# Performance work log

Hardware: AMD Instinct MI355X
Metric: run time of the kernel (lower is better)

Reference implementation:

```python
import jax, jax.numpy as jnp
import numpy as np

N, E = 100000, 1600000
NFEAT, NHID, NCLASS, NLAYER = 128, 128, 40, 3


def _glorot(key, shape):
    fan_in, fan_out = shape[0], shape[1]
    lim = float(np.sqrt(6.0 / (fan_in + fan_out)))
    return jax.random.uniform(key, shape, jnp.float32, -lim, lim)


def setup_inputs() -> dict:
    key = jax.random.key(0)
    ks = jax.random.split(key, 12)
    x = jax.random.normal(ks[0], (N, NFEAT), jnp.float32)
    src = jax.random.randint(ks[1], (E,), 0, N, jnp.int32)
    dst = jax.random.randint(ks[2], (E,), 0, N, jnp.int32)
    W1 = _glorot(ks[3], (NFEAT, NHID)); b1 = jnp.zeros((NHID,), jnp.float32)
    W2 = _glorot(ks[4], (NHID, NHID)); b2 = jnp.zeros((NHID,), jnp.float32)
    Wg = jnp.stack([_glorot(ks[5 + l], (NHID, NHID)) for l in range(NLAYER)])  # [L,H,H]
    bg = jnp.zeros((NLAYER, NHID), jnp.float32)
    Wc = _glorot(ks[5 + NLAYER], (NHID, NCLASS)); bc = jnp.zeros((NCLASS,), jnp.float32)
    return {"x": x, "src": src, "dst": dst, "W1": W1, "b1": b1, "W2": W2,
            "b2": b2, "Wg": Wg, "bg": bg, "Wc": Wc, "bc": bc}


def _graph_conv(h, src, dst, W, b, out_norm, in_norm):
    # DGL GraphConv norm='both': scale by src out-deg^{-1/2}, sum-aggregate,
    # scale by dst in-deg^{-1/2}, then linear (in_feats == out_feats -> W after agg).
    h = h * out_norm[:, None]
    agg = jax.ops.segment_sum(h[src], dst, num_segments=N)
    return (agg * in_norm[:, None]) @ W + b


def reference(x, src, dst, W1, b1, W2, b2, Wg, bg, Wc, bc):
    ones = jnp.ones((E,), jnp.float32)
    out_deg = jnp.clip(jax.ops.segment_sum(ones, src, num_segments=N), 1.0)
    in_deg = jnp.clip(jax.ops.segment_sum(ones, dst, num_segments=N), 1.0)
    out_norm = jax.lax.rsqrt(out_deg)
    in_norm = jax.lax.rsqrt(in_deg)

    h = x @ W1 + b1            # feature1
    h = h @ W2 + b2            # feature2
    for l in range(NLAYER):    # stacked GraphConv + ReLU (dropout is identity in eval)
        h = _graph_conv(h, src, dst, Wg[l], bg[l], out_norm, in_norm)
        h = jax.nn.relu(h)
    return h @ Wc + bc         # classifier
```

## Files before the change

kernel.cpp:

```cpp
#include <hip/hip_runtime.h>
#include <hip/hip_fp16.h>
#include <cstdint>
#include <cstddef>

constexpr int NN  = 100000;
constexpr int EE  = 1600000;
constexpr int HID = 128;
constexpr int BUK = 256;
constexpr int NBUK = (NN + BUK - 1) / BUK;
constexpr int BLKE = 2048;
constexpr int NBE  = (EE + BLKE - 1) / BLKE;
constexpr int MH   = NBUK * NBE;
constexpr int MH2  = 2 * MH;
constexpr int NSC  = (MH2 + 2047) / 2048;

typedef float f32x4_t __attribute__((ext_vector_type(4)));
typedef short bf16x8_t __attribute__((ext_vector_type(8)));

static __device__ __forceinline__ short f2bf(float f) {
    union { float f; unsigned u; } x; x.f = f;
    unsigned r = x.u + 0x7FFF + ((x.u >> 16) & 1);
    return (short)(r >> 16);
}
static __device__ __forceinline__ float bf2f(short b) {
    union { unsigned u; float f; } x; x.u = ((unsigned)(unsigned short)b) << 16;
    return x.f;
}

__global__ __launch_bounds__(256) void bh_both_k(const int* __restrict__ src, const int* __restrict__ dst,
                                                 int* __restrict__ bh2) {
    __shared__ int hd[NBUK], hs[NBUK];
    int blk = blockIdx.x, t = threadIdx.x;
    for (int i = t; i < NBUK; i += 256) { hd[i] = 0; hs[i] = 0; }
    __syncthreads();
    int e0 = blk * BLKE, e1 = min(e0 + BLKE, EE);
    for (int e = e0 + t; e < e1; e += 256) {
        atomicAdd(&hd[dst[e] >> 8], 1);
        atomicAdd(&hs[src[e] >> 8], 1);
    }
    __syncthreads();
    for (int i = t; i < NBUK; i += 256) {
        bh2[i * NBE + blk]      = hd[i];
        bh2[MH + i * NBE + blk] = hs[i];
    }
}

__global__ __launch_bounds__(256) void scan_sum_k(const int* __restrict__ in, int* __restrict__ bsum, int n) {
    __shared__ int sc[256];
    int b = blockIdx.x, t = threadIdx.x;
    int base = b * 2048 + t * 8;
    int s = 0;
#pragma unroll
    for (int j = 0; j < 8; j++) { int idx = base + j; s += (idx < n) ? in[idx] : 0; }
    sc[t] = s; __syncthreads();
    for (int off = 128; off > 0; off >>= 1) {
        if (t < off) sc[t] += sc[t + off];
        __syncthreads();
    }
    if (t == 0) bsum[b] = sc[0];
}

__global__ __launch_bounds__(512) void scan_top_k(const int* __restrict__ bsum, int* __restrict__ boff, int nb) {
    __shared__ int sc[512];
    int t = threadIdx.x;
    int v = (t < nb) ? bsum[t] : 0;
    sc[t] = v; __syncthreads();
    for (int off = 1; off < 512; off <<= 1) {
        int u = (t >= off) ? sc[t - off] : 0;
        __syncthreads();
        sc[t] += u;
        __syncthreads();
    }
    if (t < nb) boff[t] = sc[t] - v;
}

__global__ __launch_bounds__(256) void scan_chunk_k(const int* __restrict__ in, const int* __restrict__ boff,
                                                    int* __restrict__ out, int n) {
    __shared__ int sc[256];
    int b = blockIdx.x, t = threadIdx.x;
    int base = b * 2048 + t * 8;
    int c[8];
    int s = 0;
#pragma unroll
    for (int j = 0; j < 8; j++) { int idx = base + j; c[j] = (idx < n) ? in[idx] : 0; s += c[j]; }
    sc[t] = s; __syncthreads();
    for (int off = 1; off < 256; off <<= 1) {
        int v = (t >= off) ? sc[t - off] : 0;
        __syncthreads();
        sc[t] += v;
        __syncthreads();
    }
    int excl = sc[t] - s + boff[b];
#pragma unroll
    for (int j = 0; j < 8; j++) {
        int idx = base + j;
        if (idx < n) out[idx] = excl;
        excl += c[j];
    }
}

__global__ __launch_bounds__(256) void scatter_both_k(const int* __restrict__ src, const int* __restrict__ dst,
                                                      const int* __restrict__ off2,
                                                      unsigned* __restrict__ pairs, unsigned char* __restrict__ sbyte) {
    __shared__ int cd[NBUK], cs[NBUK];
    int blk = blockIdx.x, t = threadIdx.x;
    for (int i = t; i < NBUK; i += 256) {
        cd[i] = off2[i * NBE + blk];
        cs[i] = off2[MH + i * NBE + blk] - EE;
    }
    __syncthreads();
    int e0 = blk * BLKE, e1 = min(e0 + BLKE, EE);
    for (int e = e0 + t; e < e1; e += 256) {
        int d = dst[e], s = src[e];
        int pd = atomicAdd(&cd[d >> 8], 1);
        pairs[pd] = ((unsigned)(d & 255) << 17) | (unsigned)s;
        int ps = atomicAdd(&cs[s >> 8], 1);
        sbyte[ps] = (unsigned char)(s & 255);
    }
}

__global__ __launch_bounds__(512) void bucket_csr_ocnt_k(
    const unsigned* __restrict__ pairs, const unsigned char* __restrict__ sbyte,
    const int* __restrict__ off2,
    int* __restrict__ rowptr, int* __restrict__ col,
    float* __restrict__ inorm, float* __restrict__ onorm) {
    __shared__ int hist[BUK];
    __shared__ int excl[BUK];
    __shared__ int psum[BUK];
    int t = threadIdx.x;

    if (blockIdx.x >= NBUK) {
        int b = blockIdx.x - NBUK;
        int base = off2[MH + b * NBE] - EE;
        int endv = (b == NBUK - 1) ? EE : off2[MH + (b + 1) * NBE] - EE;
        if (t < BUK) hist[t] = 0;
        __syncthreads();
        for (int i = base + t; i < endv; i += 512) atomicAdd(&hist[sbyte[i]], 1);
        __syncthreads();
        if (t < BUK) {
            int node = b * BUK + t;
            if (node < NN) {
                int c = hist[t]; if (c < 1) c = 1;
                onorm[node] = rsqrtf((float)c);
            }
        }
        return;
    }

    int b = blockIdx.x;
    int base = off2[b * NBE];
    int endv = (b == NBUK - 1) ? EE : off2[(b + 1) * NBE];
    if (t < BUK) hist[t] = 0;
    __syncthreads();
    for (int i = base + t; i < endv; i += 512) atomicAdd(&hist[pairs[i] >> 17], 1);
    __syncthreads();
    int ps = 0;
    if (t < BUK) { ps = hist[t]; psum[t] = ps; }
    __syncthreads();
    for (int off = 1; off < BUK; off <<= 1) {
        int u = 0;
        if (t < BUK && t >= off) u = psum[t - off];
        __syncthreads();
        if (t < BUK) psum[t] += u;
        __syncthreads();
    }
    if (t < BUK) {
        int pex = psum[t] - ps;
        excl[t] = pex;
        int node = b * BUK + t;
        if (node < NN) {
            rowptr[node] = base + pex;
            int c = ps; if (c < 1) c = 1;
            inorm[node] = rsqrtf((float)c);
        }
    }
    if (b == NBUK - 1 && t == 0) rowptr[NN] = EE;
    __syncthreads();
    for (int i = base + t; i < endv; i += 512) {
        unsigned p = pairs[i];
        int pos = base + atomicAdd(&excl[p >> 17], 1);
        col[pos] = (int)(p & 0x1FFFFu);
    }
}

__global__ __launch_bounds__(256) void w12_k(const float* __restrict__ W1, const float* __restrict__ W2,
                                             const float* __restrict__ b1, const float* __restrict__ b2,
                                             const float* __restrict__ Wg,
                                             float* __restrict__ W12, float* __restrict__ b12,
                                             short* __restrict__ wsp) {
    int t = threadIdx.x;
    if (blockIdx.x == 65) {
        const float* W = Wg + 2 * 128 * 128;
        short* Bh = wsp;
        short* Bl = wsp + 16384;
        for (int j = 0; j < 16; j++) {
            int fi = (j * 256 + t) * 4;
            int k = fi >> 7, n0 = fi & 127;
            float4 wv = *(const float4*)(W + fi);
            float wa[4] = {wv.x, wv.y, wv.z, wv.w};
#pragma unroll
            for (int cc = 0; cc < 4; cc++) {
                int g = n0 + cc;
                int q2 = g >> 2;
                int ntc = q2 & 7;
                int c = ((q2 >> 3) << 2) | (g & 3);
                int kblk = k >> 5, ksub = k & 31;
                int lane_ = ((ksub >> 3) << 4) | c;
                int sidx = ((ntc * 4 + kblk) * 64 + lane_) * 8 + (ksub & 7);
                short hi = f2bf(wa[cc]);
                Bh[sidx] = hi; Bl[sidx] = f2bf(wa[cc] - bf2f(hi));
            }
        }
        return;
    }
    if (blockIdx.x == 64) {
        int j = t;
        if (j < 128) {
            float acc = b2[j];
            for (int k = 0; k < 128; k++) acc = fmaf(b1[k], W2[k * 128 + j], acc);
            b12[j] = acc;
        }
        return;
    }
    int idx = blockIdx.x * 256 + t;
    int i = idx >> 7, j = idx & 127;
    float a0 = 0.f, a1 = 0.f, a2 = 0.f, a3 = 0.f;
    for (int k = 0; k < 128; k += 4) {
        a0 = fmaf(W1[i * 128 + k],     W2[(k)     * 128 + j], a0);
        a1 = fmaf(W1[i * 128 + k + 1], W2[(k + 1) * 128 + j], a1);
        a2 = fmaf(W1[i * 128 + k + 2], W2[(k + 2) * 128 + j], a2);
        a3 = fmaf(W1[i * 128 + k + 3], W2[(k + 3) * 128 + j], a3);
    }
    W12[idx] = (a0 + a1) + (a2 + a3);
}

__global__ __launch_bounds__(256) void agg_k(const float4* __restrict__ h16, const int* __restrict__ rowptr,
                                             const int* __restrict__ col, const float* __restrict__ inorm,
                                             short* __restrict__ h0h, short* __restrict__ h0l) {
    int w = (int)((blockIdx.x * 256 + threadIdx.x) >> 6);
    if (w >= NN) return;
    int lane = threadIdx.x & 63;
    int q   = lane >> 4;
    int l16 = lane & 15;
    int beg = rowptr[w], end = rowptr[w + 1];
    float acc[8];
#pragma unroll
    for (int j = 0; j < 8; j++) acc[j] = 0.f;

    union HU { float4 f4; __half2 h2[4]; };
    int i = beg + q;
    for (; i + 12 < end; i += 16) {
        int s0 = col[i], s1 = col[i + 4], s2 = col[i + 8], s3 = col[i + 12];
        HU u0, u1, u2, u3;
        u0.f4 = h16[(size_t)s0 * 16 + l16];
        u1.f4 = h16[(size_t)s1 * 16 + l16];
        u2.f4 = h16[(size_t)s2 * 16 + l16];
        u3.f4 = h16[(size_t)s3 * 16 + l16];
#pragma unroll
        for (int p = 0; p < 4; p++) {
            float2 a = __half22float2(u0.h2[p]);
            float2 b = __half22float2(u1.h2[p]);
            float2 c = __half22float2(u2.h2[p]);
            float2 d = __half22float2(u3.h2[p]);
            acc[2 * p]     += (a.x + b.x) + (c.x + d.x);
            acc[2 * p + 1] += (a.y + b.y) + (c.y + d.y);
        }
    }
    for (; i < end; i += 4) {
        int s = col[i];
        HU u; u.f4 = h16[(size_t)s * 16 + l16];
#pragma unroll
        for (int p = 0; p < 4; p++) {
            float2 a = __half22float2(u.h2[p]);
            acc[2 * p]     += a.x;
            acc[2 * p + 1] += a.y;
        }
    }
#pragma unroll
    for (int mm = 16; mm <= 32; mm <<= 1)
#pragma unroll
        for (int j = 0; j < 8; j++) acc[j] += __shfl_xor(acc[j], mm);
    if (q == 0) {
        float s = inorm[w];
        bf16x8_t hv, lv;
#pragma unroll
        for (int j = 0; j < 8; j++) {
            float v = acc[j] * s;
            short hi = f2bf(v);
            hv[j] = hi;
            lv[j] = f2bf(v - bf2f(hi));
        }
        *(bf16x8_t*)&h0h[(size_t)w * 128 + l16 * 8] = hv;
        *(bf16x8_t*)&h0l[(size_t)w * 128 + l16 * 8] = lv;
    }
}

template <int NT, bool RELU, bool OUTSCALE, bool OUTHALF, bool INSPLIT>
__global__ __launch_bounds__(256) void mfma_gemm_k(
    const void* __restrict__ in, const short* __restrict__ inl,
    const float* __restrict__ W, const float* __restrict__ bias,
    void* __restrict__ outp, const float* __restrict__ outscale,
    int nrows, int ncols, int ntiles) {

    __shared__ short Bh[NT * 2048];
    __shared__ short Bl[NT * 2048];
    __shared__ __half Tr[OUTHALF ? 4 * 16 * 128 : 1];

    const int t = threadIdx.x;

    if constexpr (NT == 8) {
        for (int j = 0; j < 16; j++) {
            int fi = (j * 256 + t) * 4;
            int k = fi >> 7, n0 = fi & 127;
            float4 wv = *(const float4*)(W + fi);
            float wa[4] = {wv.x, wv.y, wv.z, wv.w};
#pragma unroll
            for (int cc = 0; cc < 4; cc++) {
                int g = n0 + cc;
                int q2 = g >> 2;
                int ntc = q2 & 7;
                int c = ((q2 >> 3) << 2) | (g & 3);
                int kblk = k >> 5, ksub = k & 31;
                int lane_ = ((ksub >> 3) << 4) | c;
                int sidx = ((ntc * 4 + kblk) * 64 + lane_) * 8 + (ksub & 7);
                short hi = f2bf(wa[cc]);
                Bh[sidx] = hi; Bl[sidx] = f2bf(wa[cc] - bf2f(hi));
            }
        }
    } else {
        for (int idx = t; idx < 128 * 64; idx += 256) {
            int k = idx >> 6, g = idx & 63;
            if (g < NT * 16) {
                float w = (g < 40) ? ((const float*)W)[k * 40 + g] : 0.f;
                int q2 = g >> 2;
                int ntc = q2 % NT;
                int c = (q2 / NT) * 4 + (g & 3);
                int kblk = k >> 5, ksub = k & 31;
                int lane_ = ((ksub >> 3) << 4) | c;
                int sidx = ((ntc * 4 + kblk) * 64 + lane_) * 8 + (ksub & 7);
                short hi = f2bf(w);
                Bh[sidx] = hi; Bl[sidx] = f2bf(w - bf2f(hi));
            }
        }
    }
    __syncthreads();

    const int wave = t >> 6;
    const int lane = t & 63;
    const int m    = lane & 15;
    const int kq   = lane >> 4;
    const int cbase = kq * 4 * NT;

    float bstat[4 * NT];
#pragma unroll
    for (int i = 0; i < 4 * NT; i++) {
        int g = cbase + i;
        bstat[i] = (g < ncols) ? bias[g] : 0.f;
    }

    const int wstride = gridDim.x * 4;
    for (int tile = blockIdx.x * 4 + wave; tile < ntiles; tile += wstride) {
        int row = tile * 16 + m;
        bool rv = row < nrows;

        bf16x8_t Ah[4], Al[4];
        if constexpr (INSPLIT) {
            const short* ih = (const short*)in + (size_t)row * 128 + kq * 8;
            const short* il = inl + (size_t)row * 128 + kq * 8;
#pragma unroll
            for (int kb = 0; kb < 4; kb++) {
                if (rv) {
                    Ah[kb] = *(const bf16x8_t*)(ih + kb * 32);
                    Al[kb] = *(const bf16x8_t*)(il + kb * 32);
                } else {
                    Ah[kb] = (bf16x8_t){0,0,0,0,0,0,0,0};
                    Al[kb] = (bf16x8_t){0,0,0,0,0,0,0,0};
                }
            }
        } else {
#pragma unroll
            for (int kb = 0; kb < 4; kb++) {
                const float* ap = (const float*)in + (size_t)row * 128 + kb * 32 + kq * 8;
                float4 p0, p1;
                if (rv) { p0 = *(const float4*)ap; p1 = *(const float4*)(ap + 4); }
                else    { p0 = make_float4(0,0,0,0); p1 = make_float4(0,0,0,0); }
                float av[8] = {p0.x, p0.y, p0.z, p0.w, p1.x, p1.y, p1.z, p1.w};
#pragma unroll
                for (int j = 0; j < 8; j++) {
                    float v = av[j];
                    short hi = f2bf(v);
                    Ah[kb][j] = hi;
                    Al[kb][j] = f2bf(v - bf2f(hi));
                }
            }
        }

        float osc = 1.f;
        if (OUTSCALE && rv) osc = outscale[row];

        float ov[4 * NT] __attribute__((aligned(16)));
#pragma unroll
        for (int nt = 0; nt < NT; nt++) {
            f32x4_t acc = {0.f, 0.f, 0.f, 0.f};
#pragma unroll
            for (int kb = 0; kb < 4; kb++) {
                const bf16x8_t bh = *(const bf16x8_t*)&Bh[((nt * 4 + kb) * 64 + lane) * 8];
                const bf16x8_t bl = *(const bf16x8_t*)&Bl[((nt * 4 + kb) * 64 + lane) * 8];
                acc = __builtin_amdgcn_mfma_f32_16x16x32_bf16(bh, Ah[kb], acc, 0, 0, 0);
                acc = __builtin_amdgcn_mfma_f32_16x16x32_bf16(bh, Al[kb], acc, 0, 0, 0);
                acc = __builtin_amdgcn_mfma_f32_16x16x32_bf16(bl, Ah[kb], acc, 0, 0, 0);
            }
#pragma unroll
            for (int r = 0; r < 4; r++) {
                float v = acc[r] + bstat[nt * 4 + r];
                if (RELU) v = fmaxf(v, 0.f);
                ov[nt * 4 + r] = v * osc;
            }
        }

        if constexpr (OUTHALF) {
            __half* tw = &Tr[wave * 2048];
#pragma unroll
            for (int p = 0; p < 4; p++) {
                union { __half h[8]; float4 f4; } U;
#pragma unroll
                for (int j = 0; j < 8; j++) U.h[j] = __float2half_rn(ov[p * 8 + j]);
                int bo = (cbase * 2 + p * 16) ^ ((m & 7) << 4);
                *(float4*)((char*)(tw + m * 128) + bo) = U.f4;
            }
#pragma unroll
            for (int s2 = 0; s2 < 4; s2++) {
                int r = s2 * 4 + (lane >> 4);
                int bo = ((lane & 15) * 16) ^ ((r & 7) << 4);
                float4 v = *(const float4*)((char*)(tw + r * 128) + bo);
                *(float4*)((__half*)outp + (size_t)(tile * 16 + r) * ncols + (lane & 15) * 8) = v;
            }
        } else if (rv) {
            if constexpr (NT == 8) {
                float4* p = (float4*)((float*)outp + (size_t)row * 128 + cbase);
#pragma unroll
                for (int j = 0; j < 8; j++) p[j] = ((const float4*)ov)[j];
            } else {
                float* p = (float*)outp + (size_t)row * 40 + cbase;
#pragma unroll
                for (int j = 0; j < 3; j++) {
                    if (cbase + j * 4 < 40) *(float4*)(p + j * 4) = ((const float4*)ov)[j];
                }
            }
        }
    }
}

__global__ __launch_bounds__(256) void conv_cls_k(
    const short* __restrict__ inh, const short* __restrict__ inl,
    const short* __restrict__ gBh, const short* __restrict__ gBl,
    const float* __restrict__ bg2,
    const float* __restrict__ Wc, const float* __restrict__ bc,
    float* __restrict__ out, int ntiles) {

    __shared__ short WcH[3 * 2048];
    __shared__ short WcL[3 * 2048];
    __shared__ short Lh[4][16][136];
    __shared__ short Ll[4][16][136];

    const int t = threadIdx.x;

    for (int idx = t; idx < 128 * 64; idx += 256) {
        int k = idx >> 6, g = idx & 63;
        if (g < 48) {
            float w = (g < 40) ? Wc[k * 40 + g] : 0.f;
            int q2 = g >> 2;
            int ntc = q2 % 3;
            int c = (q2 / 3) * 4 + (g & 3);
            int kblk = k >> 5, ksub = k & 31;
            int lane_ = ((ksub >> 3) << 4) | c;
            int sidx = ((ntc * 4 + kblk) * 64 + lane_) * 8 + (ksub & 7);
            short hi = f2bf(w);
            WcH[sidx] = hi; WcL[sidx] = f2bf(w - bf2f(hi));
        }
    }
    __syncthreads();

    const int wave = t >> 6;
    const int lane = t & 63;
    const int m    = lane & 15;
    const int kq   = lane >> 4;
    const int cbase = kq * 32;
    const int cbc   = kq * 12;

    float bstat[32];
#pragma unroll
    for (int i = 0; i < 32; i++) bstat[i] = bg2[cbase + i];
    float bstatC[12];
#pragma unroll
    for (int i = 0; i < 12; i++) {
        int g = cbc + i;
        bstatC[i] = (g < 40) ? bc[g] : 0.f;
    }

    const int wstride = gridDim.x * 4;
    for (int tile = blockIdx.x * 4 + wave; tile < ntiles; tile += wstride) {
        const int row = tile * 16 + m;

        bf16x8_t Ah[4], Al[4];
        {
            const short* ih = inh + (size_t)row * 128 + kq * 8;
            const short* il = inl + (size_t)row * 128 + kq * 8;
#pragma unroll
            for (int kb = 0; kb < 4; kb++) {
                Ah[kb] = *(const bf16x8_t*)(ih + kb * 32);
                Al[kb] = *(const bf16x8_t*)(il + kb * 32);
            }
        }

        float ov[32] __attribute__((aligned(16)));
#pragma unroll
        for (int nt = 0; nt < 8; nt++) {
            f32x4_t acc = {0.f, 0.f, 0.f, 0.f};
#pragma unroll
            for (int kb = 0; kb < 4; kb++) {
                const bf16x8_t bh = *(const bf16x8_t*)&gBh[((nt * 4 + kb) * 64 + lane) * 8];
                const bf16x8_t bl = *(const bf16x8_t*)&gBl[((nt * 4 + kb) * 64 + lane) * 8];
                acc = __builtin_amdgcn_mfma_f32_16x16x32_bf16(bh, Ah[kb], acc, 0, 0, 0);
                acc = __builtin_amdgcn_mfma_f32_16x16x32_bf16(bh, Al[kb], acc, 0, 0, 0);
                acc = __builtin_amdgcn_mfma_f32_16x16x32_bf16(bl, Ah[kb], acc, 0, 0, 0);
            }
#pragma unroll
            for (int r = 0; r < 4; r++) {
                float v = acc[r] + bstat[nt * 4 + r];
                ov[nt * 4 + r] = fmaxf(v, 0.f);
            }
        }

#pragma unroll
        for (int p = 0; p < 4; p++) {
            bf16x8_t hv, lv;
#pragma unroll
            for (int j = 0; j < 8; j++) {
                float v = ov[p * 8 + j];
                short hi = f2bf(v);
                hv[j] = hi;
                lv[j] = f2bf(v - bf2f(hi));
            }
            *(bf16x8_t*)&Lh[wave][m][cbase + p * 8] = hv;
            *(bf16x8_t*)&Ll[wave][m][cbase + p * 8] = lv;
        }

        float ovc[12] __attribute__((aligned(16)));
#pragma unroll
        for (int ntc = 0; ntc < 3; ntc++) {
            f32x4_t acc = {0.f, 0.f, 0.f, 0.f};
#pragma unroll
            for (int kb = 0; kb < 4; kb++) {
                const bf16x8_t wh = *(const bf16x8_t*)&WcH[((ntc * 4 + kb) * 64 + lane) * 8];
                const bf16x8_t wl = *(const bf16x8_t*)&WcL[((ntc * 4 + kb) * 64 + lane) * 8];
                const bf16x8_t fh = *(const bf16x8_t*)&Lh[wave][m][kb * 32 + kq * 8];
                const bf16x8_t fl = *(const bf16x8_t*)&Ll[wave][m][kb * 32 + kq * 8];
                acc = __builtin_amdgcn_mfma_f32_16x16x32_bf16(wh, fh, acc, 0, 0, 0);
                acc = __builtin_amdgcn_mfma_f32_16x16x32_bf16(wh, fl, acc, 0, 0, 0);
                acc = __builtin_amdgcn_mfma_f32_16x16x32_bf16(wl, fh, acc, 0, 0, 0);
            }
#pragma unroll
            for (int r = 0; r < 4; r++) ovc[ntc * 4 + r] = acc[r] + bstatC[ntc * 4 + r];
        }

        float* p = out + (size_t)row * 40 + cbc;
#pragma unroll
        for (int j = 0; j < 3; j++) {
            if (cbc + j * 4 < 40) *(float4*)(p + j * 4) = ((const float4*)ovc)[j];
        }
    }
}

extern "C" void kernel_launch(void* const* d_in, const int* in_sizes, int n_in,
                              void* d_out, int out_size, void* d_ws, size_t ws_size,
                              hipStream_t stream) {
    const float* x   = (const float*)d_in[0];
    const int*   src = (const int*)d_in[1];
    const int*   dst = (const int*)d_in[2];
    const float* W1  = (const float*)d_in[3];
    const float* b1  = (const float*)d_in[4];
    const float* W2  = (const float*)d_in[5];
    const float* b2  = (const float*)d_in[6];
    const float* Wg  = (const float*)d_in[7];
    const float* bg  = (const float*)d_in[8];
    const float* Wc  = (const float*)d_in[9];
    const float* bc  = (const float*)d_in[10];
    float* out = (float*)d_out;

    char* ws = (char*)d_ws;
    size_t off = 0;
    auto alloc = [&](size_t bytes) -> void* {
        void* p = ws + off;
        off += (bytes + 255) & ~(size_t)255;
        return p;
    };
    short*  h0h    = (short*)alloc((size_t)NN * HID * 2);
    short*  h0l    = (short*)alloc((size_t)NN * HID * 2);
    __half* h16    = (__half*)alloc((size_t)NN * HID * 2);
    float*  W12    = (float*)alloc(128 * 128 * 4);
    float*  b12    = (float*)alloc(128 * 4);
    short*  wsp    = (short*)alloc(2 * 16384 * 2);
    float*  onorm  = (float*)alloc((size_t)NN * 4);
    float*  inorm  = (float*)alloc((size_t)NN * 4);
    int*    rowptr = (int*)alloc((size_t)(NN + 1) * 4);
    int*    col    = (int*)alloc((size_t)EE * 4);
    int*    bh2    = (int*)alloc((size_t)MH2 * 4);
    int*    off2   = (int*)alloc((size_t)MH2 * 4);
    int*    bsum   = (int*)alloc((size_t)NSC * 4);
    int*    boff   = (int*)alloc((size_t)NSC * 4);
    unsigned*      pairs = (unsigned*)h0h;
    unsigned char* sbyte = (unsigned char*)h0h + (size_t)EE * 4;

    bh_both_k<<<NBE, 256, 0, stream>>>(src, dst, bh2);
    scan_sum_k<<<NSC, 256, 0, stream>>>(bh2, bsum, MH2);
    scan_top_k<<<1, 512, 0, stream>>>(bsum, boff, NSC);
    scan_chunk_k<<<NSC, 256, 0, stream>>>(bh2, boff, off2, MH2);
    scatter_both_k<<<NBE, 256, 0, stream>>>(src, dst, off2, pairs, sbyte);
    bucket_csr_ocnt_k<<<2 * NBUK, 512, 0, stream>>>(pairs, sbyte, off2,
                                                    rowptr, col, inorm, onorm);

    w12_k<<<66, 256, 0, stream>>>(W1, W2, b1, b2, Wg, W12, b12, wsp);

    const int ntiles = NN / 16;
    const int ggrid  = 512;

    mfma_gemm_k<8, false, true, true, false><<<ggrid, 256, 0, stream>>>(
        x, nullptr, W12, b12, h16, onorm, NN, 128, ntiles);
    for (int l = 0; l < 3; l++) {
        agg_k<<<(NN * 64 + 255) / 256, 256, 0, stream>>>(
            (const float4*)h16, rowptr, col, inorm, h0h, h0l);
        if (l < 2) {
            mfma_gemm_k<8, true, true, true, true><<<ggrid, 256, 0, stream>>>(
                h0h, h0l, Wg + (size_t)l * 128 * 128, bg + (size_t)l * 128, h16, onorm, NN, 128, ntiles);
        } else {
            conv_cls_k<<<ggrid, 256, 0, stream>>>(
                h0h, h0l, wsp, wsp + 16384, bg + 2 * 128, Wc, bc, out, ntiles);
        }
    }
}
```

Baseline: 534.7 us.

## Process two 16-row tiles per wave in the MFMA GEMM to reuse B fragments

The generic GEMM kernel is specialised to the 128-column fp16-output case, and each wave now handles 32 rows (two 16-row tiles) per iteration. Each B fragment read from LDS then feeds six MFMAs instead of three, which halves LDS traffic per output. The grid changes to 391 blocks with launch_bounds(256,2). In exchange register pressure rises from the doubled A fragments and accumulators, and row bounds checks are dropped, which relies on NN being divisible by 32.

```diff
diff --git a/kernel.cpp b/kernel.cpp
--- a/kernel.cpp
+++ b/kernel.cpp
@@ -295,52 +295,35 @@
     }
 }
 
-template <int NT, bool RELU, bool OUTSCALE, bool OUTHALF, bool INSPLIT>
-__global__ __launch_bounds__(256) void mfma_gemm_k(
+template <bool RELU, bool INSPLIT>
+__global__ __launch_bounds__(256, 2) void mfma_gemm2_k(
     const void* __restrict__ in, const short* __restrict__ inl,
     const float* __restrict__ W, const float* __restrict__ bias,
-    void* __restrict__ outp, const float* __restrict__ outscale,
-    int nrows, int ncols, int ntiles) {
-
-    __shared__ short Bh[NT * 2048];
-    __shared__ short Bl[NT * 2048];
-    __shared__ __half Tr[OUTHALF ? 4 * 16 * 128 : 1];
+    __half* __restrict__ outp, const float* __restrict__ outscale,
+    int nst) {
+
+    __shared__ short Bh[8 * 2048];
+    __shared__ short Bl[8 * 2048];
+    __shared__ __half Tr[4 * 16 * 128];
 
     const int t = threadIdx.x;
 
-    if constexpr (NT == 8) {
-        for (int j = 0; j < 16; j++) {
-            int fi = (j * 256 + t) * 4;
-            int k = fi >> 7, n0 = fi & 127;
-            float4 wv = *(const float4*)(W + fi);
-            float wa[4] = {wv.x, wv.y, wv.z, wv.w};
-#pragma unroll
-            for (int cc = 0; cc < 4; cc++) {
-                int g = n0 + cc;
-                int q2 = g >> 2;
-                int ntc = q2 & 7;
-                int c = ((q2 >> 3) << 2) | (g & 3);
-                int kblk = k >> 5, ksub = k & 31;
-                int lane_ = ((ksub >> 3) << 4) | c;
-                int sidx = ((ntc * 4 + kblk) * 64 + lane_) * 8 + (ksub & 7);
-                short hi = f2bf(wa[cc]);
-                Bh[sidx] = hi; Bl[sidx] = f2bf(wa[cc] - bf2f(hi));
-            }
-        }
-    } else {
-        for (int idx = t; idx < 128 * 64; idx += 256) {
-            int k = idx >> 6, g = idx & 63;
-            if (g < NT * 16) {
-                float w = (g < 40) ? ((const float*)W)[k * 40 + g] : 0.f;
-                int q2 = g >> 2;
-                int ntc = q2 % NT;
-                int c = (q2 / NT) * 4 + (g & 3);
-                int kblk = k >> 5, ksub = k & 31;
-                int lane_ = ((ksub >> 3) << 4) | c;
-                int sidx = ((ntc * 4 + kblk) * 64 + lane_) * 8 + (ksub & 7);
-                short hi = f2bf(w);
-                Bh[sidx] = hi; Bl[sidx] = f2bf(w - bf2f(hi));
-            }
+    for (int j = 0; j < 16; j++) {
+        int fi = (j * 256 + t) * 4;
+        int k = fi >> 7, n0 = fi & 127;
+        float4 wv = *(const float4*)(W + fi);
+        float wa[4] = {wv.x, wv.y, wv.z, wv.w};
+#pragma unroll
+        for (int cc = 0; cc < 4; cc++) {
+            int g = n0 + cc;
+            int q2 = g >> 2;
+            int ntc = q2 & 7;
+            int c = ((q2 >> 3) << 2) | (g & 3);
+            int kblk = k >> 5, ksub = k & 31;
+            int lane_ = ((ksub >> 3) << 4) | c;
+            int sidx = ((ntc * 4 + kblk) * 64 + lane_) * 8 + (ksub & 7);
+            short hi = f2bf(wa[cc]);
+            Bh[sidx] = hi; Bl[sidx] = f2bf(wa[cc] - bf2f(hi));
         }
     }
     __syncthreads();
@@ -349,104 +332,110 @@
     const int lane = t & 63;
     const int m    = lane & 15;
     const int kq   = lane >> 4;
-    const int cbase = kq * 4 * NT;
-
-    float bstat[4 * NT];
-#pragma unroll
-    for (int i = 0; i < 4 * NT; i++) {
-        int g = cbase + i;
-        bstat[i] = (g < ncols) ? bias[g] : 0.f;
-    }
+    const int cbase = kq * 32;
+
+    float bstat[32];
+#pragma unroll
+    for (int i = 0; i < 32; i++) bstat[i] = bias[cbase + i];
 
     const int wstride = gridDim.x * 4;
-    for (int tile = blockIdx.x * 4 + wave; tile < ntiles; tile += wstride) {
-        int row = tile * 16 + m;
-        bool rv = row < nrows;
-
-        bf16x8_t Ah[4], Al[4];
+    for (int st = blockIdx.x * 4 + wave; st < nst; st += wstride) {
+        const int row0 = st * 32 + m;
+        const int row1 = row0 + 16;
+
+        bf16x8_t A0h[4], A0l[4], A1h[4], A1l[4];
         if constexpr (INSPLIT) {
-            const short* ih = (const short*)in + (size_t)row * 128 + kq * 8;
-            const short* il = inl + (size_t)row * 128 + kq * 8;
+            const short* ih0 = (const short*)in + (size_t)row0 * 128 + kq * 8;
+            const short* il0 = inl + (size_t)row0 * 128 + kq * 8;
 #pragma unroll
             for (int kb = 0; kb < 4; kb++) {
-                if (rv) {
-                    Ah[kb] = *(const bf16x8_t*)(ih + kb * 32);
-                    Al[kb] = *(const bf16x8_t*)(il + kb * 32);
-                } else {
-                    Ah[kb] = (bf16x8_t){0,0,0,0,0,0,0,0};
-                    Al[kb] = (bf16x8_t){0,0,0,0,0,0,0,0};
+                A0h[kb] = *(const bf16x8_t*)(ih0 + kb * 32);
+                A0l[kb] = *(const bf16x8_t*)(il0 + kb * 32);
+                A1h[kb] = *(const bf16x8_t*)(ih0 + 2048 + kb * 32);
+                A1l[kb] = *(const bf16x8_t*)(il0 + 2048 + kb * 32);
+            }
+        } else {
+#pragma unroll
+            for (int kb = 0; kb < 4; kb++) {
+                const float* ap0 = (const float*)in + (size_t)row0 * 128 + kb * 32 + kq * 8;
+                float4 p0 = *(const float4*)ap0;
+                float4 p1 = *(const float4*)(ap0 + 4);
+                float4 p2 = *(const float4*)(ap0 + 2048);
+                float4 p3 = *(const float4*)(ap0 + 2048 + 4);
+                float a0v[8] = {p0.x, p0.y, p0.z, p0.w, p1.x, p1.y, p1.z, p1.w};
+                float a1v[8] = {p2.x, p2.y, p2.z, p2.w, p3.x, p3.y, p3.z, p3.w};
+#pragma unroll
+                for (int j = 0; j < 8; j++) {
+                    short h0_ = f2bf(a0v[j]);
+                    A0h[kb][j] = h0_;
+                    A0l[kb][j] = f2bf(a0v[j] - bf2f(h0_));
+                    short h1_ = f2bf(a1v[j]);
+                    A1h[kb][j] = h1_;
+                    A1l[kb][j] = f2bf(a1v[j] - bf2f(h1_));
                 }
             }
-        } else {
-#pragma unroll
-            for (int kb = 0; kb < 4; kb++) {
-                const float* ap = (const float*)in + (size_t)row * 128 + kb * 32 + kq * 8;
-                float4 p0, p1;
-                if (rv) { p0 = *(const float4*)ap; p1 = *(const float4*)(ap + 4); }
-                else    { p0 = make_float4(0,0,0,0); p1 = make_float4(0,0,0,0); }
-                float av[8] = {p0.x, p0.y, p0.z, p0.w, p1.x, p1.y, p1.z, p1.w};
-#pragma unroll
-                for (int j = 0; j < 8; j++) {
-                    float v = av[j];
-                    short hi = f2bf(v);
-                    Ah[kb][j] = hi;
-                    Al[kb][j] = f2bf(v - bf2f(hi));
-                }
-            }
-        }
-
-        float osc = 1.f;
-        if (OUTSCALE && rv) osc = outscale[row];
-
-        float ov[4 * NT] __attribute__((aligned(16)));
-#pragma unroll
-        for (int nt = 0; nt < NT; nt++) {
-            f32x4_t acc = {0.f, 0.f, 0.f, 0.f};
+        }
+
+        const float osc0 = outscale[row0];
+        const float osc1 = outscale[row1];
+
+        float ov0[32] __attribute__((aligned(16)));
+        float ov1[32] __attribute__((aligned(16)));
+#pragma unroll
+        for (int nt = 0; nt < 8; nt++) {
+            f32x4_t a0 = {0.f, 0.f, 0.f, 0.f};
+            f32x4_t a1 = {0.f, 0.f, 0.f, 0.f};
 #pragma unroll
             for (int kb = 0; kb < 4; kb++) {
                 const bf16x8_t bh = *(const bf16x8_t*)&Bh[((nt * 4 + kb) * 64 + lane) * 8];
                 const bf16x8_t bl = *(const bf16x8_t*)&Bl[((nt * 4 + kb) * 64 + lane) * 8];
-                acc = __builtin_amdgcn_mfma_f32_16x16x32_bf16(bh, Ah[kb], acc, 0, 0, 0);
-                acc = __builtin_amdgcn_mfma_f32_16x16x32_bf16(bh, Al[kb], acc, 0, 0, 0);
-                acc = __builtin_amdgcn_mfma_f32_16x16x32_bf16(bl, Ah[kb], acc, 0, 0, 0);
+                a0 = __builtin_amdgcn_mfma_f32_16x16x32_bf16(bh, A0h[kb], a0, 0, 0, 0);
+                a0 = __builtin_amdgcn_mfma_f32_16x16x32_bf16(bh, A0l[kb], a0, 0, 0, 0);
+                a0 = __builtin_amdgcn_mfma_f32_16x16x32_bf16(bl, A0h[kb], a0, 0, 0, 0);
+                a1 = __builtin_amdgcn_mfma_f32_16x16x32_bf16(bh, A1h[kb], a1, 0, 0, 0);
+                a1 = __builtin_amdgcn_mfma_f32_16x16x32_bf16(bh, A1l[kb], a1, 0, 0, 0);
+                a1 = __builtin_amdgcn_mfma_f32_16x16x32_bf16(bl, A1h[kb], a1, 0, 0, 0);
             }
 #pragma unroll
             for (int r = 0; r < 4; r++) {
-                float v = acc[r] + bstat[nt * 4 + r];
-                if (RELU) v = fmaxf(v, 0.f);
-                ov[nt * 4 + r] = v * osc;
-            }
-        }
-
-        if constexpr (OUTHALF) {
-            __half* tw = &Tr[wave * 2048];
-#pragma unroll
-            for (int p = 0; p < 4; p++) {
-                union { __half h[8]; float4 f4; } U;
-#pragma unroll
-                for (int j = 0; j < 8; j++) U.h[j] = __float2half_rn(ov[p * 8 + j]);
-                int bo = (cbase * 2 + p * 16) ^ ((m & 7) << 4);
-                *(float4*)((char*)(tw + m * 128) + bo) = U.f4;
-            }
-#pragma unroll
-            for (int s2 = 0; s2 < 4; s2++) {
-                int r = s2 * 4 + (lane >> 4);
-                int bo = ((lane & 15) * 16) ^ ((r & 7) << 4);
-                float4 v = *(const float4*)((char*)(tw + r * 128) + bo);
-                *(float4*)((__half*)outp + (size_t)(tile * 16 + r) * ncols + (lane & 15) * 8) = v;
-            }
-        } else if (rv) {
-            if constexpr (NT == 8) {
-                float4* p = (float4*)((float*)outp + (size_t)row * 128 + cbase);
-#pragma unroll
-                for (int j = 0; j < 8; j++) p[j] = ((const float4*)ov)[j];
-            } else {
-                float* p = (float*)outp + (size_t)row * 40 + cbase;
-#pragma unroll
-                for (int j = 0; j < 3; j++) {
-                    if (cbase + j * 4 < 40) *(float4*)(p + j * 4) = ((const float4*)ov)[j];
-                }
-            }
+                float v0 = a0[r] + bstat[nt * 4 + r];
+                float v1 = a1[r] + bstat[nt * 4 + r];
+                if (RELU) { v0 = fmaxf(v0, 0.f); v1 = fmaxf(v1, 0.f); }
+                ov0[nt * 4 + r] = v0 * osc0;
+                ov1[nt * 4 + r] = v1 * osc1;
+            }
+        }
+
+        __half* tw = &Tr[wave * 2048];
+#pragma unroll
+        for (int p = 0; p < 4; p++) {
+            union { __half h[8]; float4 f4; } U;
+#pragma unroll
+            for (int j = 0; j < 8; j++) U.h[j] = __float2half_rn(ov0[p * 8 + j]);
+            int bo = (cbase * 2 + p * 16) ^ ((m & 7) << 4);
+            *(float4*)((char*)(tw + m * 128) + bo) = U.f4;
+        }
+#pragma unroll
+        for (int s2 = 0; s2 < 4; s2++) {
+            int r = s2 * 4 + (lane >> 4);
+            int bo = ((lane & 15) * 16) ^ ((r & 7) << 4);
+            float4 v = *(const float4*)((char*)(tw + r * 128) + bo);
+            *(float4*)(outp + (size_t)(st * 32 + r) * 128 + (lane & 15) * 8) = v;
+        }
+#pragma unroll
+        for (int p = 0; p < 4; p++) {
+            union { __half h[8]; float4 f4; } U;
+#pragma unroll
+            for (int j = 0; j < 8; j++) U.h[j] = __float2half_rn(ov1[p * 8 + j]);
+            int bo = (cbase * 2 + p * 16) ^ ((m & 7) << 4);
+            *(float4*)((char*)(tw + m * 128) + bo) = U.f4;
+        }
+#pragma unroll
+        for (int s2 = 0; s2 < 4; s2++) {
+            int r = s2 * 4 + (lane >> 4);
+            int bo = ((lane & 15) * 16) ^ ((r & 7) << 4);
+            float4 v = *(const float4*)((char*)(tw + r * 128) + bo);
+            *(float4*)(outp + (size_t)(st * 32 + 16 + r) * 128 + (lane & 15) * 8) = v;
         }
     }
 }
@@ -623,18 +612,19 @@
     w12_k<<<66, 256, 0, stream>>>(W1, W2, b1, b2, Wg, W12, b12, wsp);
 
     const int ntiles = NN / 16;
-    const int ggrid  = 512;
-
-    mfma_gemm_k<8, false, true, true, false><<<ggrid, 256, 0, stream>>>(
-        x, nullptr, W12, b12, h16, onorm, NN, 128, ntiles);
+    const int nst    = NN / 32;
+    const int g2grid = 391;
+
+    mfma_gemm2_k<false, false><<<g2grid, 256, 0, stream>>>(
+        x, nullptr, W12, b12, h16, onorm, nst);
     for (int l = 0; l < 3; l++) {
         agg_k<<<(NN * 64 + 255) / 256, 256, 0, stream>>>(
             (const float4*)h16, rowptr, col, inorm, h0h, h0l);
         if (l < 2) {
-            mfma_gemm_k<8, true, true, true, true><<<ggrid, 256, 0, stream>>>(
-                h0h, h0l, Wg + (size_t)l * 128 * 128, bg + (size_t)l * 128, h16, onorm, NN, 128, ntiles);
+            mfma_gemm2_k<true, true><<<g2grid, 256, 0, stream>>>(
+                h0h, h0l, Wg + (size_t)l * 128 * 128, bg + (size_t)l * 128, h16, onorm, nst);
         } else {
-            conv_cls_k<<<ggrid, 256, 0, stream>>>(
+            conv_cls_k<<<512, 256, 0, stream>>>(
                 h0h, h0l, wsp, wsp + 16384, bg + 2 * 128, Wc, bc, out, ntiles);
         }
     }
```

Measured after the change: 626.6 us. +17.2%, slower.
